# Kernel tuning notes

Measured on AMD Instinct MI355X. Metric: run time of the kernel, lower is better.

Reference implementation:

```python
import jax, jax.numpy as jnp
import numpy as np


def _edge_index(n):
    # all ordered pairs (i, j), i != j -- static since n is a Python int
    ii = np.repeat(np.arange(n), n)
    jj = np.tile(np.arange(n), n)
    m = ii != jj
    return jnp.asarray(ii[m]), jnp.asarray(jj[m])


def _mlp2(x, w1, b1, w2, b2):
    # two Linear layers with ReLU after each (PointNet-style MLP([a,b,c]))
    h = jax.nn.relu(x @ w1 + b1)
    return jax.nn.relu(h @ w2 + b2)


def _fcn(x, w1, b1, w2, b2, w3, b3):
    # FullyConnectedNet: relu(fc1) -> relu(fc2) -> fc3 (no final relu)
    h = jax.nn.relu(x @ w1 + b1)
    h = jax.nn.relu(h @ w2 + b2)
    return h @ w3 + b3


def setup_inputs() -> dict:
    key = jax.random.key(0)
    ks = jax.random.split(key, 32)
    n = 256
    E = n * (n - 1)
    d = 512

    def lin(k, fin, fout):
        k1, k2 = jax.random.split(k)
        s = 1.0 / np.sqrt(fin)
        w = jax.random.uniform(k1, (fin, fout), jnp.float32, -s, s)
        b = jax.random.uniform(k2, (fout,), jnp.float32, -s, s)
        return w, b

    inp = {
        "insnum": n,
        "pred_codes": jax.random.normal(ks[0], (E, d), jnp.float32),
        "bboxes": jax.random.normal(ks[1], (n, 2, 3), jnp.float32),
        "lwhV": jax.random.uniform(ks[2], (n, 3), jnp.float32),
        "centroid": jax.random.normal(ks[3], (n, 3), jnp.float32),
    }
    inp["s_w1"], inp["s_b1"] = lin(ks[4], 512, 512)
    inp["s_w2"], inp["s_b2"] = lin(ks[5], 512, 512)
    inp["p_w1"], inp["p_b1"] = lin(ks[6], 512 + 128, 512)
    inp["p_w2"], inp["p_b2"] = lin(ks[7], 512, 512)
    inp["c_w1"], inp["c_b1"] = lin(ks[8], 512, 512)
    inp["c_w2"], inp["c_b2"] = lin(ks[9], 512, 512)
    inp["l_w1"], inp["l_b1"] = lin(ks[10], 512 * 3, 512)
    inp["l_w2"], inp["l_b2"] = lin(ks[11], 512, 512)
    inp["pos_w1"], inp["pos_b1"] = lin(ks[12], 5, 64)
    inp["pos_w2"], inp["pos_b2"] = lin(ks[13], 64, 64)
    inp["pos_w3"], inp["pos_b3"] = lin(ks[14], 64, 128)
    return inp


def reference(insnum, pred_codes, bboxes, lwhV, centroid,
              s_w1, s_b1, s_w2, s_b2,
              p_w1, p_b1, p_w2, p_b2,
              c_w1, c_b1, c_w2, c_b2,
              l_w1, l_b1, l_w2, l_b2,
              pos_w1, pos_b1, pos_w2, pos_b2, pos_w3, pos_b3):
    src, dst = _edge_index(insnum)
    ci = centroid[src, :2]          # [E, 2]
    cj = centroid[dst, :2]          # [E, 2]
    diff = ci - cj                  # vectorized replacement of per-edge loop
    distance = jnp.linalg.norm(diff, axis=1, keepdims=True)   # [E, 1]
    direction = diff / distance                                # [E, 2]
    pos_features = jnp.concatenate([diff, distance, direction], axis=1)  # [E, 5]

    support_codes = _mlp2(pred_codes, s_w1, s_b1, s_w2, s_b2)
    pos_codes = _fcn(pos_features, pos_w1, pos_b1, pos_w2, pos_b2, pos_w3, pos_b3)
    proximity_features = jnp.concatenate([pred_codes, pos_codes], axis=1)  # [E, 640]
    proximity_codes = _mlp2(proximity_features, p_w1, p_b1, p_w2, p_b2)
    comp_codes = _mlp2(pred_codes, c_w1, c_b1, c_w2, c_b2)
    link_in = jnp.concatenate([support_codes, proximity_codes, comp_codes], axis=1)  # [E, 1536]
    link_codes = _mlp2(link_in, l_w1, l_b1, l_w2, l_b2)
    return (link_codes, support_codes, proximity_codes, comp_codes)
```

## Files before the change

kernel.cpp:

```cpp
#include <hip/hip_runtime.h>
#include <stdint.h>

typedef unsigned short ushort_t;
typedef __attribute__((ext_vector_type(8))) short short8;
typedef __attribute__((ext_vector_type(8))) unsigned short u16x8;
typedef __attribute__((ext_vector_type(4))) float f32x4;

#define GLOBAL_AS __attribute__((address_space(1)))
#define LDS_AS __attribute__((address_space(3)))

__device__ __forceinline__ ushort_t f2bf(float f) {
  union { float f; uint32_t u; } v; v.f = f;
  uint32_t u = v.u;
  u += 0x7FFFu + ((u >> 16) & 1u);
  return (ushort_t)(u >> 16);
}

__device__ __forceinline__ int swz(int row, int byteInRow) {
  return (row * 128 + byteInRow) ^ ((row & 7) << 4);
}

struct TransArgs {
  const float* src[8];
  ushort_t* dst[8];
  int K[8];
  int blk0[9];
};

__global__ __launch_bounds__(256) void transpose_weights(TransArgs ta) {
  __shared__ float tile[64 * 65];
  int b = blockIdx.x;
  int mi = 0;
#pragma unroll
  for (int i = 1; i < 8; ++i) if (b >= ta.blk0[i]) mi = i;
  const float* src = ta.src[mi];
  ushort_t* dst = ta.dst[mi];
  int K = ta.K[mi];
  int rel = b - ta.blk0[mi];
  int ktiles = K >> 6;
  int k0 = (rel % ktiles) << 6;
  int n0 = (rel / ktiles) << 6;
  int t = threadIdx.x;
#pragma unroll
  for (int i = 0; i < 16; ++i) {
    int idx = i * 256 + t;
    int r = idx >> 6, c = idx & 63;
    tile[r * 65 + c] = src[(size_t)(k0 + r) * 512 + (n0 + c)];
  }
  __syncthreads();
#pragma unroll
  for (int i = 0; i < 16; ++i) {
    int idx = i * 256 + t;
    int r = idx >> 6, c = idx & 63;
    dst[(size_t)(n0 + r) * K + (k0 + c)] = f2bf(tile[c * 65 + r]);
  }
}

__global__ __launch_bounds__(256) void prep_kernel(
    const float* __restrict__ pred, const float* __restrict__ centroid,
    const float* __restrict__ pw1, const float* __restrict__ pb1,
    const float* __restrict__ pw2, const float* __restrict__ pb2,
    const float* __restrict__ pw3, const float* __restrict__ pb3,
    ushort_t* __restrict__ X, ushort_t* __restrict__ pos, int nm1)
{
  __shared__ ushort_t h1s[128 * 64];
  __shared__ ushort_t h2s[128 * 64];
  __shared__ ushort_t w2t[64 * 64];
  __shared__ ushort_t w3t[128 * 64];
  __shared__ float w1s[5 * 64];
  __shared__ float b1s[64], b2s[64], b3s[128];
  int t = threadIdx.x;
  for (int idx = t; idx < 64 * 64; idx += 256) {
    int k = idx >> 6, n = idx & 63;
    *(ushort_t*)((char*)w2t + swz(n, k * 2)) = f2bf(pw2[idx]);
  }
  for (int idx = t; idx < 64 * 128; idx += 256) {
    int k = idx >> 7, n = idx & 127;
    *(ushort_t*)((char*)w3t + swz(n, k * 2)) = f2bf(pw3[idx]);
  }
  for (int i = t; i < 5 * 64; i += 256) w1s[i] = pw1[i];
  if (t < 64) { b1s[t] = pb1[t]; b2s[t] = pb2[t]; }
  if (t < 128) b3s[t] = pb3[t];
  __syncthreads();

  int wid = t >> 6, lane = t & 63;
  int ebase = blockIdx.x * 128 + wid * 32;
  for (int it = 0; it < 32; ++it) {
    int e = ebase + it;
    const float* pr = pred + (size_t)e * 512 + lane * 8;
    float4 pA = *(const float4*)pr;
    float4 pB = *(const float4*)(pr + 4);
    u16x8 o;
    o[0] = f2bf(pA.x); o[1] = f2bf(pA.y); o[2] = f2bf(pA.z); o[3] = f2bf(pA.w);
    o[4] = f2bf(pB.x); o[5] = f2bf(pB.y); o[6] = f2bf(pB.z); o[7] = f2bf(pB.w);
    *(u16x8*)(X + (size_t)e * 512 + lane * 8) = o;
    int i = e / nm1;
    int r = e - i * nm1;
    int j = r + (r >= i ? 1 : 0);
    float dx = centroid[i * 3 + 0] - centroid[j * 3 + 0];
    float dy = centroid[i * 3 + 1] - centroid[j * 3 + 1];
    float dist = sqrtf(dx * dx + dy * dy);
    float inv = 1.0f / dist;
    float h1 = w1s[0 * 64 + lane] * dx + w1s[1 * 64 + lane] * dy + w1s[2 * 64 + lane] * dist
             + w1s[3 * 64 + lane] * (dx * inv) + w1s[4 * 64 + lane] * (dy * inv) + b1s[lane];
    h1 = fmaxf(h1, 0.0f);
    int row = wid * 32 + it;
    *(ushort_t*)((char*)h1s + swz(row, lane * 2)) = f2bf(h1);
  }
  __syncthreads();

  int colg = lane & 15, rowg = (lane >> 4) << 2;
  int ko_lane = (lane >> 4) * 8;
  {
    f32x4 acc[2][4];
    f32x4 zero = {0.0f, 0.0f, 0.0f, 0.0f};
#pragma unroll
    for (int m_ = 0; m_ < 2; ++m_)
#pragma unroll
      for (int n_ = 0; n_ < 4; ++n_) acc[m_][n_] = zero;
#pragma unroll
    for (int kk = 0; kk < 2; ++kk) {
      int ko = kk * 32 + ko_lane;
      short8 a[2], b[4];
#pragma unroll
      for (int m_ = 0; m_ < 2; ++m_)
        a[m_] = *(const short8*)((const char*)h1s + swz(wid * 32 + m_ * 16 + colg, ko * 2));
#pragma unroll
      for (int n_ = 0; n_ < 4; ++n_)
        b[n_] = *(const short8*)((const char*)w2t + swz(n_ * 16 + colg, ko * 2));
#pragma unroll
      for (int m_ = 0; m_ < 2; ++m_)
#pragma unroll
        for (int n_ = 0; n_ < 4; ++n_)
          acc[m_][n_] = __builtin_amdgcn_mfma_f32_16x16x32_bf16(a[m_], b[n_], acc[m_][n_], 0, 0, 0);
    }
#pragma unroll
    for (int n_ = 0; n_ < 4; ++n_) {
      int col = n_ * 16 + colg;
      float bv = b2s[col];
#pragma unroll
      for (int m_ = 0; m_ < 2; ++m_) {
        int row = wid * 32 + m_ * 16 + rowg;
#pragma unroll
        for (int jj = 0; jj < 4; ++jj) {
          float v = fmaxf(acc[m_][n_][jj] + bv, 0.0f);
          *(ushort_t*)((char*)h2s + swz(row + jj, col * 2)) = f2bf(v);
        }
      }
    }
  }
  __syncthreads();
  {
    f32x4 acc[2][8];
    f32x4 zero = {0.0f, 0.0f, 0.0f, 0.0f};
#pragma unroll
    for (int m_ = 0; m_ < 2; ++m_)
#pragma unroll
      for (int n_ = 0; n_ < 8; ++n_) acc[m_][n_] = zero;
#pragma unroll
    for (int kk = 0; kk < 2; ++kk) {
      int ko = kk * 32 + ko_lane;
      short8 a[2], b[8];
#pragma unroll
      for (int m_ = 0; m_ < 2; ++m_)
        a[m_] = *(const short8*)((const char*)h2s + swz(wid * 32 + m_ * 16 + colg, ko * 2));
#pragma unroll
      for (int n_ = 0; n_ < 8; ++n_)
        b[n_] = *(const short8*)((const char*)w3t + swz(n_ * 16 + colg, ko * 2));
#pragma unroll
      for (int m_ = 0; m_ < 2; ++m_)
#pragma unroll
        for (int n_ = 0; n_ < 8; ++n_)
          acc[m_][n_] = __builtin_amdgcn_mfma_f32_16x16x32_bf16(a[m_], b[n_], acc[m_][n_], 0, 0, 0);
    }
#pragma unroll
    for (int n_ = 0; n_ < 8; ++n_) {
      int col = n_ * 16 + colg;
      float bv = b3s[col];
#pragma unroll
      for (int m_ = 0; m_ < 2; ++m_) {
        int row = wid * 32 + m_ * 16 + rowg;
#pragma unroll
        for (int jj = 0; jj < 4; ++jj) {
          int e = blockIdx.x * 128 + row + jj;
          pos[(size_t)e * 128 + col] = f2bf(acc[m_][n_][jj] + bv);
        }
      }
    }
  }
}

__global__ __launch_bounds__(256) void gemm_bias_relu(
    const void* __restrict__ A0, int lda0,
    const void* __restrict__ A1, int lda1,
    const void* __restrict__ A2, int lda2,
    int s0, int s1, int aF32,
    const ushort_t* __restrict__ Bt, const float* __restrict__ bias,
    void* __restrict__ Cout, int outF32, ushort_t* __restrict__ Cdual, int K)
{
  __shared__ ushort_t As[128 * 64];
  __shared__ ushort_t Bs[128 * 64];
  int bid = blockIdx.x;
  int cpx = gridDim.x >> 3;
  int swzb = (bid & 7) * cpx + (bid >> 3);
  int mt = swzb >> 2, nt = swzb & 3;
  int m0 = mt << 7, n0 = nt << 7;
  int t = threadIdx.x;
  int lane = t & 63, wid = t >> 6;
  int wm = wid >> 1, wn = wid & 1;
  f32x4 acc[4][4];
  f32x4 zero = {0.0f, 0.0f, 0.0f, 0.0f};
#pragma unroll
  for (int a_ = 0; a_ < 4; ++a_)
#pragma unroll
    for (int b_ = 0; b_ < 4; ++b_) acc[a_][b_] = zero;

  for (int kt = 0; kt < K; kt += 64) {
    const void* Ab; int ldaA; int kin;
    if (kt < s0)      { Ab = A0; ldaA = lda0; kin = kt; }
    else if (kt < s1) { Ab = A1; ldaA = lda1; kin = kt - s0; }
    else              { Ab = A2; ldaA = lda2; kin = kt - s1; }
    if (aF32) {
      const float* Af = (const float*)Ab;
      int rr = t >> 1, cc0 = (t & 1) << 5;
      const float* g = Af + (size_t)(m0 + rr) * ldaA + kin + cc0;
      ushort_t* ldst = As + rr * 64 + cc0;
#pragma unroll
      for (int i = 0; i < 4; ++i) {
        float4 v0 = *(const float4*)(g + i * 8);
        float4 v1 = *(const float4*)(g + i * 8 + 4);
        u16x8 o;
        o[0] = f2bf(v0.x); o[1] = f2bf(v0.y); o[2] = f2bf(v0.z); o[3] = f2bf(v0.w);
        o[4] = f2bf(v1.x); o[5] = f2bf(v1.y); o[6] = f2bf(v1.z); o[7] = f2bf(v1.w);
        *(u16x8*)(ldst + i * 8) = o;
      }
    } else {
      const ushort_t* Ah = (const ushort_t*)Ab;
#pragma unroll
      for (int i = 0; i < 4; ++i) {
        int ch = i * 256 + t;
        int rr = ch >> 3, cc = (ch & 7) << 3;
        const ushort_t* g = Ah + (size_t)(m0 + rr) * ldaA + kin + cc;
        __builtin_amdgcn_global_load_lds((const GLOBAL_AS void*)g,
                                         (LDS_AS void*)(As + ch * 8), 16, 0, 0);
      }
    }
#pragma unroll
    for (int i = 0; i < 4; ++i) {
      int ch = i * 256 + t;
      int rr = ch >> 3, cc = (ch & 7) << 3;
      const ushort_t* g = Bt + (size_t)(n0 + rr) * K + kt + cc;
      __builtin_amdgcn_global_load_lds((const GLOBAL_AS void*)g,
                                       (LDS_AS void*)(Bs + ch * 8), 16, 0, 0);
    }
    __syncthreads();
#pragma unroll
    for (int kk = 0; kk < 64; kk += 32) {
      int ko = kk + (lane >> 4) * 8;
      short8 a[4], b[4];
#pragma unroll
      for (int m_ = 0; m_ < 4; ++m_)
        a[m_] = *(const short8*)(As + (wm * 64 + m_ * 16 + (lane & 15)) * 64 + ko);
#pragma unroll
      for (int n_ = 0; n_ < 4; ++n_)
        b[n_] = *(const short8*)(Bs + (wn * 64 + n_ * 16 + (lane & 15)) * 64 + ko);
#pragma unroll
      for (int m_ = 0; m_ < 4; ++m_)
#pragma unroll
        for (int n_ = 0; n_ < 4; ++n_)
          acc[m_][n_] = __builtin_amdgcn_mfma_f32_16x16x32_bf16(a[m_], b[n_], acc[m_][n_], 0, 0, 0);
    }
    __syncthreads();
  }
  int colg = lane & 15, rowg = (lane >> 4) << 2;
  float* C32 = (float*)Cout;
  ushort_t* C16 = (ushort_t*)Cout;
#pragma unroll
  for (int n_ = 0; n_ < 4; ++n_) {
    int col = n0 + wn * 64 + n_ * 16 + colg;
    float bv = bias[col];
#pragma unroll
    for (int m_ = 0; m_ < 4; ++m_) {
      int row = m0 + wm * 64 + m_ * 16 + rowg;
#pragma unroll
      for (int jj = 0; jj < 4; ++jj) {
        float v = fmaxf(acc[m_][n_][jj] + bv, 0.0f);
        if (outF32) C32[(size_t)(row + jj) * 512 + col] = v;
        else        C16[(size_t)(row + jj) * 512 + col] = f2bf(v);
        if (Cdual)  Cdual[(size_t)(row + jj) * 512 + col] = f2bf(v);
      }
    }
  }
}

__global__ __launch_bounds__(512) void gemm256_bias_relu(
    const ushort_t* __restrict__ A0, int lda0,
    const ushort_t* __restrict__ A1, int lda1,
    const ushort_t* __restrict__ A2, int lda2,
    int s0, int s1,
    const ushort_t* __restrict__ Bt, const float* __restrict__ bias,
    void* __restrict__ Cout, int outF32, ushort_t* __restrict__ Cdual, int K)
{
  __shared__ ushort_t As[4 * 8192];
  __shared__ ushort_t Bs[4 * 8192];
  int bid = blockIdx.x;
  int nwg = gridDim.x;
  int q = nwg >> 3, r8 = nwg & 7;
  int xcd = bid & 7, ii = bid >> 3;
  int sid = (xcd < r8 ? xcd * (q + 1) : r8 * (q + 1) + (xcd - r8) * q) + ii;
  int mt = sid >> 1, nt = sid & 1;
  int m0 = mt << 8, n0 = nt << 8;
  int t = threadIdx.x;
  int lane = t & 63, wid = t >> 6;
  int wm = wid >> 2, wn = wid & 3;
  int l15 = lane & 15;
  int kb = (lane >> 4) << 4;
  int sw = (l15 & 3) << 4;
  int NT = K >> 5;

  f32x4 acc[8][4];
  f32x4 zero = {0.0f, 0.0f, 0.0f, 0.0f};
#pragma unroll
  for (int mf = 0; mf < 8; ++mf)
#pragma unroll
    for (int nf = 0; nf < 4; ++nf) acc[mf][nf] = zero;

  int rA = t >> 2;
  int cq = (t & 3) << 4;

  auto stage = [&](int tile) {
    int kt = tile << 5;
    const ushort_t* Ap; int ld; int kin;
    if (kt < s0)      { Ap = A0; ld = lda0; kin = kt; }
    else if (kt < s1) { Ap = A1; ld = lda1; kin = kt - s0; }
    else              { Ap = A2; ld = lda2; kin = kt - s1; }
    ushort_t* Ad = As + (size_t)(tile & 3) * 8192;
    ushort_t* Bd = Bs + (size_t)(tile & 3) * 8192;
#pragma unroll
    for (int h = 0; h < 2; ++h) {
      int row = h * 128 + rA;
      int cb = cq ^ ((row & 3) << 4);
      const ushort_t* g = Ap + (size_t)(m0 + row) * ld + kin + (cb >> 1);
      __builtin_amdgcn_global_load_lds((const GLOBAL_AS void*)g,
          (LDS_AS void*)(Ad + h * 4096 + t * 8), 16, 0, 0);
    }
#pragma unroll
    for (int h = 0; h < 2; ++h) {
      int row = h * 128 + rA;
      int cb = cq ^ ((row & 3) << 4);
      const ushort_t* g = Bt + (size_t)(n0 + row) * K + kt + (cb >> 1);
      __builtin_amdgcn_global_load_lds((const GLOBAL_AS void*)g,
          (LDS_AS void*)(Bd + h * 4096 + t * 8), 16, 0, 0);
    }
  };

  stage(0); stage(1); stage(2);
  asm volatile("s_waitcnt vmcnt(8)" ::: "memory");
  __builtin_amdgcn_s_barrier();
  __builtin_amdgcn_sched_barrier(0);

  for (int tt = 0; tt < NT; ++tt) {
    if (tt + 3 < NT) stage(tt + 3);
    const char* Ab_ = (const char*)(As + (size_t)(tt & 3) * 8192);
    const char* Bb_ = (const char*)(Bs + (size_t)(tt & 3) * 8192);
    short8 b[4];
#pragma unroll
    for (int nf = 0; nf < 4; ++nf) {
      int row = wn * 64 + nf * 16 + l15;
      b[nf] = *(const short8*)(Bb_ + row * 64 + (kb ^ sw));
    }
    __builtin_amdgcn_s_setprio(1);
#pragma unroll
    for (int mf = 0; mf < 8; ++mf) {
      int row = wm * 128 + mf * 16 + l15;
      short8 a = *(const short8*)(Ab_ + row * 64 + (kb ^ sw));
#pragma unroll
      for (int nf = 0; nf < 4; ++nf)
        acc[mf][nf] = __builtin_amdgcn_mfma_f32_16x16x32_bf16(a, b[nf], acc[mf][nf], 0, 0, 0);
    }
    __builtin_amdgcn_s_setprio(0);
    __builtin_amdgcn_sched_barrier(0);
    if (tt + 3 < NT)      asm volatile("s_waitcnt vmcnt(8)" ::: "memory");
    else if (tt + 2 < NT) asm volatile("s_waitcnt vmcnt(4)" ::: "memory");
    else if (tt + 1 < NT) asm volatile("s_waitcnt vmcnt(0)" ::: "memory");
    __builtin_amdgcn_s_barrier();
    __builtin_amdgcn_sched_barrier(0);
  }

  int colg = l15, rowg = (lane >> 4) << 2;
  float* C32 = (float*)Cout;
  ushort_t* C16 = (ushort_t*)Cout;
#pragma unroll
  for (int nf = 0; nf < 4; ++nf) {
    int col = n0 + wn * 64 + nf * 16 + colg;
    float bv = bias[col];
#pragma unroll
    for (int mf = 0; mf < 8; ++mf) {
      int row = m0 + wm * 128 + mf * 16 + rowg;
#pragma unroll
      for (int jj = 0; jj < 4; ++jj) {
        float v = fmaxf(acc[mf][nf][jj] + bv, 0.0f);
        if (outF32) C32[(size_t)(row + jj) * 512 + col] = v;
        else        C16[(size_t)(row + jj) * 512 + col] = f2bf(v);
        if (Cdual)  Cdual[(size_t)(row + jj) * 512 + col] = f2bf(v);
      }
    }
  }
}

extern "C" void kernel_launch(void* const* d_in, const int* in_sizes, int n_in,
                              void* d_out, int out_size, void* d_ws, size_t ws_size,
                              hipStream_t stream) {
  (void)n_in; (void)out_size;
  const float* pred = (const float*)d_in[1];
  const float* centroid = (const float*)d_in[4];
  const float* W[8] = { (const float*)d_in[5],  (const float*)d_in[7],  (const float*)d_in[9],
                        (const float*)d_in[11], (const float*)d_in[13], (const float*)d_in[15],
                        (const float*)d_in[17], (const float*)d_in[19] };
  const float* Bv[8] = { (const float*)d_in[6],  (const float*)d_in[8],  (const float*)d_in[10],
                         (const float*)d_in[12], (const float*)d_in[14], (const float*)d_in[16],
                         (const float*)d_in[18], (const float*)d_in[20] };
  int Kd[8] = {512, 512, 640, 512, 512, 512, 1536, 512};
  const float* pos_w1 = (const float*)d_in[21]; const float* pos_b1 = (const float*)d_in[22];
  const float* pos_w2 = (const float*)d_in[23]; const float* pos_b2 = (const float*)d_in[24];
  const float* pos_w3 = (const float*)d_in[25]; const float* pos_b3 = (const float*)d_in[26];

  int E = in_sizes[1] / 512;
  int n = in_sizes[4] / 3;

  char* ws = (char*)d_ws;
  size_t off = 0;
  auto alloc = [&](size_t bytes) -> void* {
    void* p = ws + off;
    off = (off + bytes + 255) & ~(size_t)255;
    return p;
  };
  size_t SB = (size_t)E * 512 * 2;
  ushort_t* Wt[8];
  for (int i = 0; i < 8; ++i) Wt[i] = (ushort_t*)alloc((size_t)Kd[i] * 512 * 2);
  ushort_t* X = (ushort_t*)alloc(SB);
  ushort_t* Hb_ws    = (ushort_t*)alloc(SB);
  ushort_t* sup16_ws = (ushort_t*)alloc(SB);
  bool fast = (off <= ws_size) && (E % 256 == 0);

  float* outF = (float*)d_out;
  size_t S = (size_t)E * 512;
  float* out_link = outF;
  float* out_sup  = outF + S;
  float* out_prox = outF + 2 * S;
  float* out_comp = outF + 3 * S;
  ushort_t* pos = (ushort_t*)d_out;

  TransArgs ta;
  int nblk = 0;
  for (int i = 0; i < 8; ++i) {
    ta.src[i] = W[i]; ta.dst[i] = Wt[i]; ta.K[i] = Kd[i];
    ta.blk0[i] = nblk;
    nblk += (Kd[i] >> 6) * 8;
  }
  ta.blk0[8] = nblk;
  hipLaunchKernelGGL(transpose_weights, dim3(nblk), dim3(256), 0, stream, ta);
  hipLaunchKernelGGL(prep_kernel, dim3(E / 128), dim3(256), 0, stream,
                     pred, centroid, pos_w1, pos_b1, pos_w2, pos_b2, pos_w3, pos_b3,
                     X, pos, n - 1);

  const ushort_t* Zu = nullptr;
  ushort_t* NO16 = nullptr;

  if (fast) {
    dim3 g256(E / 256 * 2), b256(512);
    ushort_t* prox16 = (ushort_t*)d_out;
    ushort_t* comp16 = X;
    ushort_t* Hl = Hb_ws;
    hipLaunchKernelGGL(gemm256_bias_relu, g256, b256, 0, stream,
                       (const ushort_t*)X, 512, (const ushort_t*)pos, 128, Zu, 0, 512, 640,
                       Wt[2], Bv[2], (void*)Hb_ws, 0, NO16, 640);
    hipLaunchKernelGGL(gemm256_bias_relu, g256, b256, 0, stream,
                       (const ushort_t*)Hb_ws, 512, Zu, 0, Zu, 0, 512, 512,
                       Wt[3], Bv[3], (void*)out_prox, 1, prox16, 512);
    hipLaunchKernelGGL(gemm256_bias_relu, g256, b256, 0, stream,
                       (const ushort_t*)X, 512, Zu, 0, Zu, 0, 512, 512,
                       Wt[0], Bv[0], (void*)Hb_ws, 0, NO16, 512);
    hipLaunchKernelGGL(gemm256_bias_relu, g256, b256, 0, stream,
                       (const ushort_t*)Hb_ws, 512, Zu, 0, Zu, 0, 512, 512,
                       Wt[1], Bv[1], (void*)out_sup, 1, sup16_ws, 512);
    hipLaunchKernelGGL(gemm256_bias_relu, g256, b256, 0, stream,
                       (const ushort_t*)X, 512, Zu, 0, Zu, 0, 512, 512,
                       Wt[4], Bv[4], (void*)Hb_ws, 0, NO16, 512);
    hipLaunchKernelGGL(gemm256_bias_relu, g256, b256, 0, stream,
                       (const ushort_t*)Hb_ws, 512, Zu, 0, Zu, 0, 512, 512,
                       Wt[5], Bv[5], (void*)out_comp, 1, comp16, 512);
    hipLaunchKernelGGL(gemm256_bias_relu, g256, b256, 0, stream,
                       (const ushort_t*)sup16_ws, 512, (const ushort_t*)prox16, 512,
                       (const ushort_t*)comp16, 512, 512, 1024,
                       Wt[6], Bv[6], (void*)Hl, 0, NO16, 1536);
    hipLaunchKernelGGL(gemm256_bias_relu, g256, b256, 0, stream,
                       (const ushort_t*)Hl, 512, Zu, 0, Zu, 0, 512, 512,
                       Wt[7], Bv[7], (void*)out_link, 1, NO16, 512);
  } else {
    dim3 g(E / 128 * 4), blk(256);
    const void* Z = nullptr;
    ushort_t* Hb = (ushort_t*)((char*)d_out + (size_t)32 * 1024 * 1024);
    ushort_t* Hl = X;
    hipLaunchKernelGGL(gemm_bias_relu, g, blk, 0, stream,
                       (const void*)X, 512, (const void*)pos, 128, Z, 0, 512, 640, 0,
                       Wt[2], Bv[2], (void*)Hb, 0, NO16, 640);
    hipLaunchKernelGGL(gemm_bias_relu, g, blk, 0, stream,
                       (const void*)Hb, 512, Z, 0, Z, 0, 512, 512, 0,
                       Wt[3], Bv[3], (void*)out_prox, 1, NO16, 512);
    hipLaunchKernelGGL(gemm_bias_relu, g, blk, 0, stream,
                       (const void*)X, 512, Z, 0, Z, 0, 512, 512, 0,
                       Wt[0], Bv[0], (void*)Hb, 0, NO16, 512);
    hipLaunchKernelGGL(gemm_bias_relu, g, blk, 0, stream,
                       (const void*)Hb, 512, Z, 0, Z, 0, 512, 512, 0,
                       Wt[1], Bv[1], (void*)out_sup, 1, NO16, 512);
    hipLaunchKernelGGL(gemm_bias_relu, g, blk, 0, stream,
                       (const void*)X, 512, Z, 0, Z, 0, 512, 512, 0,
                       Wt[4], Bv[4], (void*)Hb, 0, NO16, 512);
    hipLaunchKernelGGL(gemm_bias_relu, g, blk, 0, stream,
                       (const void*)Hb, 512, Z, 0, Z, 0, 512, 512, 0,
                       Wt[5], Bv[5], (void*)out_comp, 1, NO16, 512);
    hipLaunchKernelGGL(gemm_bias_relu, g, blk, 0, stream,
                       (const void*)out_sup, 512, (const void*)out_prox, 512,
                       (const void*)out_comp, 512, 512, 1024, 1,
                       Wt[6], Bv[6], (void*)Hl, 0, NO16, 1536);
    hipLaunchKernelGGL(gemm_bias_relu, g, blk, 0, stream,
                       (const void*)Hl, 512, Z, 0, Z, 0, 512, 512, 0,
                       Wt[7], Bv[7], (void*)out_link, 1, NO16, 512);
  }
}
```

Baseline: 885.1 us.

## Rewrite 256x256 GEMM as 8-phase double-buffered pipeline with BK=64

Replaces the 4-stage BK=32 GEMM mainloop with a BK=64 double-buffered schedule. Each K tile is split into four phases, and every phase interleaves LDS fragment reads, one half-tile global-to-LDS load and an MFMA burst, with barriers between phases. The aim is to spread memory issue evenly across compute and to widen the per-row LDS layout to 128 bytes with an XOR swizzle, reducing bank conflicts and waitcnt stalls. It raises LDS use to 128KB per block and adds more barriers per tile, which may hurt if the synchronisation overhead dominates.

```diff
diff --git a/kernel.cpp b/kernel.cpp
--- a/kernel.cpp
+++ b/kernel.cpp
@@ -293,7 +293,51 @@
   }
 }
 
-__global__ __launch_bounds__(512) void gemm256_bias_relu(
+template<int Q, class F>
+__device__ __forceinline__ void phase_op(
+    const char* As_, const char* Bs_, int tile,
+    int wm, int wn, int g, int l15,
+    short8 (&bfr)[4][2], f32x4 (&acc)[8][4], F&& doStage, int vm)
+{
+  int db = tile & 1;
+  const char* Ab = As_ + db * 32768 + wm * 16384;
+  const char* Bb = Bs_ + db * 32768 + (wn >> 1) * 16384;
+  if (Q == 0) {
+#pragma unroll
+    for (int nf = 0; nf < 4; ++nf) {
+      int rb = ((wn & 1) << 6) + nf * 16 + l15;
+      int sb = (rb & 7) << 4;
+      bfr[nf][0] = *(const short8*)(Bb + rb * 128 + ((g * 16) ^ sb));
+      bfr[nf][1] = *(const short8*)(Bb + rb * 128 + ((64 + g * 16) ^ sb));
+    }
+  }
+  int ra0 = (2 * Q) * 16 + l15, ra1 = (2 * Q + 1) * 16 + l15;
+  int sa0 = (ra0 & 7) << 4, sa1 = (ra1 & 7) << 4;
+  short8 a00 = *(const short8*)(Ab + ra0 * 128 + ((g * 16) ^ sa0));
+  short8 a01 = *(const short8*)(Ab + ra0 * 128 + ((64 + g * 16) ^ sa0));
+  short8 a10 = *(const short8*)(Ab + ra1 * 128 + ((g * 16) ^ sa1));
+  short8 a11 = *(const short8*)(Ab + ra1 * 128 + ((64 + g * 16) ^ sa1));
+  doStage();
+  __builtin_amdgcn_s_barrier();
+  asm volatile("s_waitcnt lgkmcnt(0)" ::: "memory");
+  __builtin_amdgcn_sched_barrier(0);
+  __builtin_amdgcn_s_setprio(1);
+#pragma unroll
+  for (int nf = 0; nf < 4; ++nf) {
+    acc[2 * Q][nf]     = __builtin_amdgcn_mfma_f32_16x16x32_bf16(a00, bfr[nf][0], acc[2 * Q][nf], 0, 0, 0);
+    acc[2 * Q][nf]     = __builtin_amdgcn_mfma_f32_16x16x32_bf16(a01, bfr[nf][1], acc[2 * Q][nf], 0, 0, 0);
+    acc[2 * Q + 1][nf] = __builtin_amdgcn_mfma_f32_16x16x32_bf16(a10, bfr[nf][0], acc[2 * Q + 1][nf], 0, 0, 0);
+    acc[2 * Q + 1][nf] = __builtin_amdgcn_mfma_f32_16x16x32_bf16(a11, bfr[nf][1], acc[2 * Q + 1][nf], 0, 0, 0);
+  }
+  __builtin_amdgcn_s_setprio(0);
+  __builtin_amdgcn_sched_barrier(0);
+  if (vm == 1)      { asm volatile("s_waitcnt vmcnt(4)" ::: "memory"); }
+  else if (vm == 2) { asm volatile("s_waitcnt vmcnt(0)" ::: "memory"); }
+  __builtin_amdgcn_s_barrier();
+  __builtin_amdgcn_sched_barrier(0);
+}
+
+__global__ __launch_bounds__(512) void gemm256_8ph(
     const ushort_t* __restrict__ A0, int lda0,
     const ushort_t* __restrict__ A1, int lda1,
     const ushort_t* __restrict__ A2, int lda2,
@@ -301,8 +345,8 @@
     const ushort_t* __restrict__ Bt, const float* __restrict__ bias,
     void* __restrict__ Cout, int outF32, ushort_t* __restrict__ Cdual, int K)
 {
-  __shared__ ushort_t As[4 * 8192];
-  __shared__ ushort_t Bs[4 * 8192];
+  __shared__ char As[65536];
+  __shared__ char Bs[65536];
   int bid = blockIdx.x;
   int nwg = gridDim.x;
   int q = nwg >> 3, r8 = nwg & 7;
@@ -311,12 +355,10 @@
   int mt = sid >> 1, nt = sid & 1;
   int m0 = mt << 8, n0 = nt << 8;
   int t = threadIdx.x;
-  int lane = t & 63, wid = t >> 6;
+  int lane = t & 63;
+  int wid = t >> 6;
   int wm = wid >> 2, wn = wid & 3;
-  int l15 = lane & 15;
-  int kb = (lane >> 4) << 4;
-  int sw = (l15 & 3) << 4;
-  int NT = K >> 5;
+  int g = lane >> 4, l15 = lane & 15;
 
   f32x4 acc[8][4];
   f32x4 zero = {0.0f, 0.0f, 0.0f, 0.0f};
@@ -324,70 +366,53 @@
   for (int mf = 0; mf < 8; ++mf)
 #pragma unroll
     for (int nf = 0; nf < 4; ++nf) acc[mf][nf] = zero;
-
-  int rA = t >> 2;
-  int cq = (t & 3) << 4;
-
-  auto stage = [&](int tile) {
-    int kt = tile << 5;
-    const ushort_t* Ap; int ld; int kin;
-    if (kt < s0)      { Ap = A0; ld = lda0; kin = kt; }
-    else if (kt < s1) { Ap = A1; ld = lda1; kin = kt - s0; }
-    else              { Ap = A2; ld = lda2; kin = kt - s1; }
-    ushort_t* Ad = As + (size_t)(tile & 3) * 8192;
-    ushort_t* Bd = Bs + (size_t)(tile & 3) * 8192;
-#pragma unroll
-    for (int h = 0; h < 2; ++h) {
-      int row = h * 128 + rA;
-      int cb = cq ^ ((row & 3) << 4);
-      const ushort_t* g = Ap + (size_t)(m0 + row) * ld + kin + (cb >> 1);
-      __builtin_amdgcn_global_load_lds((const GLOBAL_AS void*)g,
-          (LDS_AS void*)(Ad + h * 4096 + t * 8), 16, 0, 0);
-    }
-#pragma unroll
-    for (int h = 0; h < 2; ++h) {
-      int row = h * 128 + rA;
-      int cb = cq ^ ((row & 3) << 4);
-      const ushort_t* g = Bt + (size_t)(n0 + row) * K + kt + (cb >> 1);
-      __builtin_amdgcn_global_load_lds((const GLOBAL_AS void*)g,
-          (LDS_AS void*)(Bd + h * 4096 + t * 8), 16, 0, 0);
+  short8 bfr[4][2];
+
+  auto stageHalf = [&](int tile, int isB, int h) {
+    int kt = tile << 6;
+    int db = tile & 1;
+    char* dst = (isB ? (char*)Bs : (char*)As) + db * 32768 + h * 16384 + wid * 2048;
+    const ushort_t* src; int ld; int kin; int r0;
+    if (isB) { src = Bt; ld = K; kin = kt; r0 = n0 + h * 128; }
+    else {
+      if (kt < s0)      { src = A0; ld = lda0; kin = kt; }
+      else if (kt < s1) { src = A1; ld = lda1; kin = kt - s0; }
+      else              { src = A2; ld = lda2; kin = kt - s1; }
+      r0 = m0 + h * 128;
+    }
+#pragma unroll
+    for (int L = 0; L < 2; ++L) {
+      int c = wid * 128 + L * 64 + lane;
+      int row = c >> 3;
+      int sl = (c & 7) ^ (row & 7);
+      const ushort_t* gp = src + (size_t)(r0 + row) * ld + kin + sl * 8;
+      __builtin_amdgcn_global_load_lds((const GLOBAL_AS void*)gp,
+          (LDS_AS void*)(dst + L * 1024 + lane * 16), 16, 0, 0);
     }
   };
 
-  stage(0); stage(1); stage(2);
-  asm volatile("s_waitcnt vmcnt(8)" ::: "memory");
+  stageHalf(0, 0, 0); stageHalf(0, 0, 1);
+  stageHalf(0, 1, 0); stageHalf(0, 1, 1);
+  stageHalf(1, 1, 0); stageHalf(1, 1, 1);
+  asm volatile("s_waitcnt vmcnt(0)" ::: "memory");
   __builtin_amdgcn_s_barrier();
   __builtin_amdgcn_sched_barrier(0);
 
-  for (int tt = 0; tt < NT; ++tt) {
-    if (tt + 3 < NT) stage(tt + 3);
-    const char* Ab_ = (const char*)(As + (size_t)(tt & 3) * 8192);
-    const char* Bb_ = (const char*)(Bs + (size_t)(tt & 3) * 8192);
-    short8 b[4];
-#pragma unroll
-    for (int nf = 0; nf < 4; ++nf) {
-      int row = wn * 64 + nf * 16 + l15;
-      b[nf] = *(const short8*)(Bb_ + row * 64 + (kb ^ sw));
-    }
-    __builtin_amdgcn_s_setprio(1);
-#pragma unroll
-    for (int mf = 0; mf < 8; ++mf) {
-      int row = wm * 128 + mf * 16 + l15;
-      short8 a = *(const short8*)(Ab_ + row * 64 + (kb ^ sw));
-#pragma unroll
-      for (int nf = 0; nf < 4; ++nf)
-        acc[mf][nf] = __builtin_amdgcn_mfma_f32_16x16x32_bf16(a, b[nf], acc[mf][nf], 0, 0, 0);
-    }
-    __builtin_amdgcn_s_setprio(0);
-    __builtin_amdgcn_sched_barrier(0);
-    if (tt + 3 < NT)      asm volatile("s_waitcnt vmcnt(8)" ::: "memory");
-    else if (tt + 2 < NT) asm volatile("s_waitcnt vmcnt(4)" ::: "memory");
-    else if (tt + 1 < NT) asm volatile("s_waitcnt vmcnt(0)" ::: "memory");
-    __builtin_amdgcn_s_barrier();
-    __builtin_amdgcn_sched_barrier(0);
-  }
-
-  int colg = l15, rowg = (lane >> 4) << 2;
+  int NT = K >> 6, NI = NT >> 1;
+  for (int j = 0; j < NI; ++j) {
+    int u = 2 * j, v = u + 1, u2 = u + 2, v2 = v + 2;
+    bool full = (u2 < NT);
+    phase_op<0>(As, Bs, u, wm, wn, g, l15, bfr, acc, [&] { stageHalf(v, 0, 0); }, 0);
+    phase_op<1>(As, Bs, u, wm, wn, g, l15, bfr, acc, [&] { stageHalf(v, 0, 1); }, 0);
+    phase_op<2>(As, Bs, u, wm, wn, g, l15, bfr, acc, [&] { if (full) stageHalf(u2, 1, 0); }, 0);
+    phase_op<3>(As, Bs, u, wm, wn, g, l15, bfr, acc, [&] { if (full) stageHalf(u2, 1, 1); }, full ? 1 : 2);
+    phase_op<0>(As, Bs, v, wm, wn, g, l15, bfr, acc, [&] { if (full) stageHalf(u2, 0, 0); }, 0);
+    phase_op<1>(As, Bs, v, wm, wn, g, l15, bfr, acc, [&] { if (full) stageHalf(u2, 0, 1); }, 0);
+    phase_op<2>(As, Bs, v, wm, wn, g, l15, bfr, acc, [&] { if (full) stageHalf(v2, 1, 0); }, 0);
+    phase_op<3>(As, Bs, v, wm, wn, g, l15, bfr, acc, [&] { if (full) stageHalf(v2, 1, 1); }, full ? 1 : 2);
+  }
+
+  int colg = l15, rowg = g << 2;
   float* C32 = (float*)Cout;
   ushort_t* C16 = (ushort_t*)Cout;
 #pragma unroll
@@ -472,29 +497,29 @@
     ushort_t* prox16 = (ushort_t*)d_out;
     ushort_t* comp16 = X;
     ushort_t* Hl = Hb_ws;
-    hipLaunchKernelGGL(gemm256_bias_relu, g256, b256, 0, stream,
+    hipLaunchKernelGGL(gemm256_8ph, g256, b256, 0, stream,
                        (const ushort_t*)X, 512, (const ushort_t*)pos, 128, Zu, 0, 512, 640,
                        Wt[2], Bv[2], (void*)Hb_ws, 0, NO16, 640);
-    hipLaunchKernelGGL(gemm256_bias_relu, g256, b256, 0, stream,
+    hipLaunchKernelGGL(gemm256_8ph, g256, b256, 0, stream,
                        (const ushort_t*)Hb_ws, 512, Zu, 0, Zu, 0, 512, 512,
                        Wt[3], Bv[3], (void*)out_prox, 1, prox16, 512);
-    hipLaunchKernelGGL(gemm256_bias_relu, g256, b256, 0, stream,
+    hipLaunchKernelGGL(gemm256_8ph, g256, b256, 0, stream,
                        (const ushort_t*)X, 512, Zu, 0, Zu, 0, 512, 512,
                        Wt[0], Bv[0], (void*)Hb_ws, 0, NO16, 512);
-    hipLaunchKernelGGL(gemm256_bias_relu, g256, b256, 0, stream,
+    hipLaunchKernelGGL(gemm256_8ph, g256, b256, 0, stream,
                        (const ushort_t*)Hb_ws, 512, Zu, 0, Zu, 0, 512, 512,
                        Wt[1], Bv[1], (void*)out_sup, 1, sup16_ws, 512);
-    hipLaunchKernelGGL(gemm256_bias_relu, g256, b256, 0, stream,
+    hipLaunchKernelGGL(gemm256_8ph, g256, b256, 0, stream,
                        (const ushort_t*)X, 512, Zu, 0, Zu, 0, 512, 512,
                        Wt[4], Bv[4], (void*)Hb_ws, 0, NO16, 512);
-    hipLaunchKernelGGL(gemm256_bias_relu, g256, b256, 0, stream,
+    hipLaunchKernelGGL(gemm256_8ph, g256, b256, 0, stream,
                        (const ushort_t*)Hb_ws, 512, Zu, 0, Zu, 0, 512, 512,
                        Wt[5], Bv[5], (void*)out_comp, 1, comp16, 512);
-    hipLaunchKernelGGL(gemm256_bias_relu, g256, b256, 0, stream,
+    hipLaunchKernelGGL(gemm256_8ph, g256, b256, 0, stream,
                        (const ushort_t*)sup16_ws, 512, (const ushort_t*)prox16, 512,
                        (const ushort_t*)comp16, 512, 512, 1024,
                        Wt[6], Bv[6], (void*)Hl, 0, NO16, 1536);
-    hipLaunchKernelGGL(gemm256_bias_relu, g256, b256, 0, stream,
+    hipLaunchKernelGGL(gemm256_8ph, g256, b256, 0, stream,
                        (const ushort_t*)Hl, 512, Zu, 0, Zu, 0, 512, 512,
                        Wt[7], Bv[7], (void*)out_link, 1, NO16, 512);
   } else {
```

Result: faster. 773.4 us (-12.6%).

## Shrink GEMM tile to 128x256 with double buffering and higher occupancy

Applied to the files above, without the earlier changes.

Replaces the 256x256 tile GEMM, which used a 4-stage LDS pipeline, with a 128x256 tile using a 2-stage double buffer and launch bounds that request 4 blocks per CU. Each wave now holds a 4x4 accumulator set instead of 8x4, which lowers register and LDS use so more waves can be resident. The grid doubles and the fast path now only needs E divisible by 128. The trade-off is less data reuse per tile and a shallower prefetch depth, so global memory latency may be less well hidden.

```diff
diff --git a/kernel.cpp b/kernel.cpp
--- a/kernel.cpp
+++ b/kernel.cpp
@@ -293,7 +293,7 @@
   }
 }
 
-__global__ __launch_bounds__(512) void gemm256_bias_relu(
+__global__ __launch_bounds__(512, 4) void gemm128_bk32(
     const ushort_t* __restrict__ A0, int lda0,
     const ushort_t* __restrict__ A1, int lda1,
     const ushort_t* __restrict__ A2, int lda2,
@@ -301,93 +301,94 @@
     const ushort_t* __restrict__ Bt, const float* __restrict__ bias,
     void* __restrict__ Cout, int outF32, ushort_t* __restrict__ Cdual, int K)
 {
-  __shared__ ushort_t As[4 * 8192];
-  __shared__ ushort_t Bs[4 * 8192];
+  __shared__ char As[2 * 8192];
+  __shared__ char Bs[2 * 16384];
   int bid = blockIdx.x;
   int nwg = gridDim.x;
-  int q = nwg >> 3, r8 = nwg & 7;
+  int q = nwg >> 3, r8_ = nwg & 7;
   int xcd = bid & 7, ii = bid >> 3;
-  int sid = (xcd < r8 ? xcd * (q + 1) : r8 * (q + 1) + (xcd - r8) * q) + ii;
+  int sid = (xcd < r8_ ? xcd * (q + 1) : r8_ * (q + 1) + (xcd - r8_) * q) + ii;
   int mt = sid >> 1, nt = sid & 1;
-  int m0 = mt << 8, n0 = nt << 8;
+  int m0 = mt << 7, n0 = nt << 8;
   int t = threadIdx.x;
   int lane = t & 63, wid = t >> 6;
   int wm = wid >> 2, wn = wid & 3;
-  int l15 = lane & 15;
-  int kb = (lane >> 4) << 4;
-  int sw = (l15 & 3) << 4;
-  int NT = K >> 5;
-
-  f32x4 acc[8][4];
+  int g = lane >> 4, l15 = lane & 15;
+
+  f32x4 acc[4][4];
   f32x4 zero = {0.0f, 0.0f, 0.0f, 0.0f};
 #pragma unroll
-  for (int mf = 0; mf < 8; ++mf)
+  for (int mf = 0; mf < 4; ++mf)
 #pragma unroll
     for (int nf = 0; nf < 4; ++nf) acc[mf][nf] = zero;
-
-  int rA = t >> 2;
-  int cq = (t & 3) << 4;
 
   auto stage = [&](int tile) {
     int kt = tile << 5;
-    const ushort_t* Ap; int ld; int kin;
-    if (kt < s0)      { Ap = A0; ld = lda0; kin = kt; }
-    else if (kt < s1) { Ap = A1; ld = lda1; kin = kt - s0; }
-    else              { Ap = A2; ld = lda2; kin = kt - s1; }
-    ushort_t* Ad = As + (size_t)(tile & 3) * 8192;
-    ushort_t* Bd = Bs + (size_t)(tile & 3) * 8192;
-#pragma unroll
-    for (int h = 0; h < 2; ++h) {
-      int row = h * 128 + rA;
-      int cb = cq ^ ((row & 3) << 4);
-      const ushort_t* g = Ap + (size_t)(m0 + row) * ld + kin + (cb >> 1);
-      __builtin_amdgcn_global_load_lds((const GLOBAL_AS void*)g,
-          (LDS_AS void*)(Ad + h * 4096 + t * 8), 16, 0, 0);
-    }
-#pragma unroll
-    for (int h = 0; h < 2; ++h) {
-      int row = h * 128 + rA;
-      int cb = cq ^ ((row & 3) << 4);
-      const ushort_t* g = Bt + (size_t)(n0 + row) * K + kt + (cb >> 1);
-      __builtin_amdgcn_global_load_lds((const GLOBAL_AS void*)g,
-          (LDS_AS void*)(Bd + h * 4096 + t * 8), 16, 0, 0);
+    const ushort_t* src; int ld; int kin;
+    if (kt < s0)      { src = A0; ld = lda0; kin = kt; }
+    else if (kt < s1) { src = A1; ld = lda1; kin = kt - s0; }
+    else              { src = A2; ld = lda2; kin = kt - s1; }
+    char* Ad = As + (tile & 1) * 8192;
+    {
+      int c = t;
+      int row = c >> 2;
+      int sl = (c & 3) ^ (row & 3);
+      const ushort_t* gp = src + (size_t)(m0 + row) * ld + kin + sl * 8;
+      __builtin_amdgcn_global_load_lds((const GLOBAL_AS void*)gp,
+          (LDS_AS void*)(Ad + c * 16), 16, 0, 0);
+    }
+    char* Bd = Bs + (tile & 1) * 16384;
+#pragma unroll
+    for (int L = 0; L < 2; ++L) {
+      int c = wid * 128 + L * 64 + lane;
+      int row = c >> 2;
+      int sl = (c & 3) ^ (row & 3);
+      const ushort_t* gp = Bt + (size_t)(n0 + row) * K + kt + sl * 8;
+      __builtin_amdgcn_global_load_lds((const GLOBAL_AS void*)gp,
+          (LDS_AS void*)(Bd + c * 16), 16, 0, 0);
     }
   };
 
-  stage(0); stage(1); stage(2);
-  asm volatile("s_waitcnt vmcnt(8)" ::: "memory");
+  stage(0);
+  asm volatile("s_waitcnt vmcnt(0)" ::: "memory");
   __builtin_amdgcn_s_barrier();
   __builtin_amdgcn_sched_barrier(0);
 
+  int NT = K >> 5;
   for (int tt = 0; tt < NT; ++tt) {
-    if (tt + 3 < NT) stage(tt + 3);
-    const char* Ab_ = (const char*)(As + (size_t)(tt & 3) * 8192);
-    const char* Bb_ = (const char*)(Bs + (size_t)(tt & 3) * 8192);
-    short8 b[4];
+    if (tt + 1 < NT) {
+      stage(tt + 1);
+      asm volatile("s_waitcnt vmcnt(3)" ::: "memory");
+    } else {
+      asm volatile("s_waitcnt vmcnt(0)" ::: "memory");
+    }
+    __builtin_amdgcn_s_barrier();
+    __builtin_amdgcn_sched_barrier(0);
+    const char* Ab = As + (tt & 1) * 8192;
+    const char* Bb = Bs + (tt & 1) * 16384;
+    short8 a[4], b[4];
 #pragma unroll
     for (int nf = 0; nf < 4; ++nf) {
-      int row = wn * 64 + nf * 16 + l15;
-      b[nf] = *(const short8*)(Bb_ + row * 64 + (kb ^ sw));
+      int r = wn * 64 + nf * 16 + l15;
+      b[nf] = *(const short8*)(Bb + r * 64 + ((g * 16) ^ ((r & 3) << 4)));
+    }
+#pragma unroll
+    for (int mf = 0; mf < 4; ++mf) {
+      int r = wm * 64 + mf * 16 + l15;
+      a[mf] = *(const short8*)(Ab + r * 64 + ((g * 16) ^ ((r & 3) << 4)));
     }
     __builtin_amdgcn_s_setprio(1);
 #pragma unroll
-    for (int mf = 0; mf < 8; ++mf) {
-      int row = wm * 128 + mf * 16 + l15;
-      short8 a = *(const short8*)(Ab_ + row * 64 + (kb ^ sw));
+    for (int mf = 0; mf < 4; ++mf)
 #pragma unroll
       for (int nf = 0; nf < 4; ++nf)
-        acc[mf][nf] = __builtin_amdgcn_mfma_f32_16x16x32_bf16(a, b[nf], acc[mf][nf], 0, 0, 0);
-    }
+        acc[mf][nf] = __builtin_amdgcn_mfma_f32_16x16x32_bf16(a[mf], b[nf], acc[mf][nf], 0, 0, 0);
     __builtin_amdgcn_s_setprio(0);
     __builtin_amdgcn_sched_barrier(0);
-    if (tt + 3 < NT)      asm volatile("s_waitcnt vmcnt(8)" ::: "memory");
-    else if (tt + 2 < NT) asm volatile("s_waitcnt vmcnt(4)" ::: "memory");
-    else if (tt + 1 < NT) asm volatile("s_waitcnt vmcnt(0)" ::: "memory");
     __builtin_amdgcn_s_barrier();
-    __builtin_amdgcn_sched_barrier(0);
-  }
-
-  int colg = l15, rowg = (lane >> 4) << 2;
+  }
+
+  int colg = l15, rowg = g << 2;
   float* C32 = (float*)Cout;
   ushort_t* C16 = (ushort_t*)Cout;
 #pragma unroll
@@ -395,8 +396,8 @@
     int col = n0 + wn * 64 + nf * 16 + colg;
     float bv = bias[col];
 #pragma unroll
-    for (int mf = 0; mf < 8; ++mf) {
-      int row = m0 + wm * 128 + mf * 16 + rowg;
+    for (int mf = 0; mf < 4; ++mf) {
+      int row = m0 + wm * 64 + mf * 16 + rowg;
 #pragma unroll
       for (int jj = 0; jj < 4; ++jj) {
         float v = fmaxf(acc[mf][nf][jj] + bv, 0.0f);
@@ -441,7 +442,7 @@
   ushort_t* X = (ushort_t*)alloc(SB);
   ushort_t* Hb_ws    = (ushort_t*)alloc(SB);
   ushort_t* sup16_ws = (ushort_t*)alloc(SB);
-  bool fast = (off <= ws_size) && (E % 256 == 0);
+  bool fast = (off <= ws_size) && (E % 128 == 0);
 
   float* outF = (float*)d_out;
   size_t S = (size_t)E * 512;
@@ -468,33 +469,33 @@
   ushort_t* NO16 = nullptr;
 
   if (fast) {
-    dim3 g256(E / 256 * 2), b256(512);
+    dim3 g128(E / 128 * 2), b512(512);
     ushort_t* prox16 = (ushort_t*)d_out;
     ushort_t* comp16 = X;
     ushort_t* Hl = Hb_ws;
-    hipLaunchKernelGGL(gemm256_bias_relu, g256, b256, 0, stream,
+    hipLaunchKernelGGL(gemm128_bk32, g128, b512, 0, stream,
                        (const ushort_t*)X, 512, (const ushort_t*)pos, 128, Zu, 0, 512, 640,
                        Wt[2], Bv[2], (void*)Hb_ws, 0, NO16, 640);
-    hipLaunchKernelGGL(gemm256_bias_relu, g256, b256, 0, stream,
+    hipLaunchKernelGGL(gemm128_bk32, g128, b512, 0, stream,
                        (const ushort_t*)Hb_ws, 512, Zu, 0, Zu, 0, 512, 512,
                        Wt[3], Bv[3], (void*)out_prox, 1, prox16, 512);
-    hipLaunchKernelGGL(gemm256_bias_relu, g256, b256, 0, stream,
+    hipLaunchKernelGGL(gemm128_bk32, g128, b512, 0, stream,
                        (const ushort_t*)X, 512, Zu, 0, Zu, 0, 512, 512,
                        Wt[0], Bv[0], (void*)Hb_ws, 0, NO16, 512);
-    hipLaunchKernelGGL(gemm256_bias_relu, g256, b256, 0, stream,
+    hipLaunchKernelGGL(gemm128_bk32, g128, b512, 0, stream,
                        (const ushort_t*)Hb_ws, 512, Zu, 0, Zu, 0, 512, 512,
                        Wt[1], Bv[1], (void*)out_sup, 1, sup16_ws, 512);
-    hipLaunchKernelGGL(gemm256_bias_relu, g256, b256, 0, stream,
+    hipLaunchKernelGGL(gemm128_bk32, g128, b512, 0, stream,
                        (const ushort_t*)X, 512, Zu, 0, Zu, 0, 512, 512,
                        Wt[4], Bv[4], (void*)Hb_ws, 0, NO16, 512);
-    hipLaunchKernelGGL(gemm256_bias_relu, g256, b256, 0, stream,
+    hipLaunchKernelGGL(gemm128_bk32, g128, b512, 0, stream,
                        (const ushort_t*)Hb_ws, 512, Zu, 0, Zu, 0, 512, 512,
                        Wt[5], Bv[5], (void*)out_comp, 1, comp16, 512);
-    hipLaunchKernelGGL(gemm256_bias_relu, g256, b256, 0, stream,
+    hipLaunchKernelGGL(gemm128_bk32, g128, b512, 0, stream,
                        (const ushort_t*)sup16_ws, 512, (const ushort_t*)prox16, 512,
                        (const ushort_t*)comp16, 512, 512, 1024,
                        Wt[6], Bv[6], (void*)Hl, 0, NO16, 1536);
-    hipLaunchKernelGGL(gemm256_bias_relu, g256, b256, 0, stream,
+    hipLaunchKernelGGL(gemm128_bk32, g128, b512, 0, stream,
                        (const ushort_t*)Hl, 512, Zu, 0, Zu, 0, 512, 512,
                        Wt[7], Bv[7], (void*)out_link, 1, NO16, 512);
   } else {
```

Measured after the change: 770.5 us. -12.9%, faster.
